# Optimization experiments

Measured on AMD Instinct MI355X. Metric: run time of the kernel, lower is better.

The kernel has to match this reference:

```python
import jax, jax.numpy as jnp
import numpy as np

# ---- static config (from xib add_argument defaults / chosen production sizes) ----
B, L = 16, 50            # batch, text length
LU, KU, DIM = 60, 100, 60
V, MAXVL = 2000, 10      # vocab size, max vocab word length (J)
MIN_WL, MAX_WL = 4, 10   # min/max extracted word length
NE = MAX_WL - MIN_WL + 1 # number of len_e candidates
INS_DEL_COST = 3.5       # min_ins_del_cost
UNEXTRACTED_PROB = 0.01
CONTEXT_WEIGHT = 0.1     # weight for context (conv) log-probs
NEG = -9999.9


def setup_inputs() -> dict:
    key = jax.random.key(0)
    ks = jax.random.split(key, 8)
    unit_id_seqs = jax.random.randint(ks[0], (B, L), 0, LU)
    lengths = 10 + jax.random.randint(ks[1], (B,), 0, L - 9)  # in [10, L]
    unit_repr = jax.random.normal(ks[2], (KU, DIM), jnp.float32)
    aligner_weight = 0.1 * jax.random.normal(ks[3], (LU, KU), jnp.float32)
    conv_w = jax.random.normal(ks[4], (DIM, DIM, 3), jnp.float32) / np.sqrt(3.0 * DIM)
    conv_b = jnp.zeros((DIM,), jnp.float32)
    vocab_ids = jax.random.randint(ks[5], (V, MAXVL), 0, KU)
    vocab_lengths = MIN_WL + jax.random.randint(ks[6], (V,), 0, MAXVL - MIN_WL + 1)
    return dict(unit_id_seqs=unit_id_seqs, lengths=lengths, unit_repr=unit_repr,
                aligner_weight=aligner_weight, conv_w=conv_w, conv_b=conv_b,
                vocab_ids=vocab_ids, vocab_lengths=vocab_lengths)


def reference(unit_id_seqs, lengths, unit_repr, aligner_weight, conv_w, conv_b,
              vocab_ids, vocab_lengths):
    # ---- G2P layer: embedding-as-matmul + Conv1d over length ----
    ku_char_repr = aligner_weight @ unit_repr                 # (LU, DIM)
    emb = ku_char_repr[unit_id_seqs]                          # (B, L, DIM)
    x = jnp.swapaxes(emb, 1, 2)                               # (B, DIM, L)
    y = jax.lax.conv_general_dilated(x, conv_w, (1,), 'SAME',
                                     dimension_numbers=('NCH', 'OIH', 'NCH'))
    word_repr = jnp.swapaxes(y + conv_b[None, :, None], 1, 2)  # (B, L, DIM)
    char_log_probs = jax.nn.log_softmax(ku_char_repr @ unit_repr.T, axis=-1)  # (LU, KU)
    alignment = jnp.exp(char_log_probs)
    ctx_log_probs = jax.nn.log_softmax(word_repr @ unit_repr.T, axis=-1)      # (B, L, KU)
    # per-position substitution log prob against each known unit
    pos_lp = char_log_probs[unit_id_seqs] + CONTEXT_WEIGHT * ctx_log_probs    # (B, L, KU)
    sub = pos_lp[:, :, vocab_ids]                                             # (B, L, V, J)
    sub = jnp.pad(sub, ((0, 0), (0, MAX_WL), (0, 0), (0, 0)), constant_values=NEG)
    J = MAXVL
    # ---- edit-distance style DP over (span char i, vocab char j), vectorized
    # over (batch, start position, vocab). prev[b,s,j,v] = f[i-1][j].
    j_ar = jnp.arange(J + 1, dtype=sub.dtype)
    prev = jnp.broadcast_to((-INS_DEL_COST * j_ar)[None, None, :, None], (B, L, J + 1, V))
    vl_idx = jnp.broadcast_to(vocab_lengths[None, None, None, :].astype(jnp.int32), (B, L, 1, V))
    lls = []
    for i in range(1, MAX_WL + 1):          # fixed small loop (<=10)
        sub_i = sub[:, i - 1:i - 1 + L]     # (B, L, V, J): char at position s+i-1
        row = [jnp.full((B, L, V), -INS_DEL_COST * i, dtype=sub.dtype)]
        for j in range(1, J + 1):           # fixed small loop (<=10)
            diag = prev[:, :, j - 1, :] + sub_i[:, :, :, j - 1]
            up = prev[:, :, j, :] - INS_DEL_COST
            left = row[j - 1] - INS_DEL_COST
            row.append(jnp.maximum(diag, jnp.maximum(up, left)))
        prev = jnp.stack(row, axis=2)       # (B, L, J+1, V)
        if i >= MIN_WL:                     # matched ll for word length i
            lls.append(jnp.take_along_axis(prev, vl_idx, axis=2)[:, :, 0, :])
    ll = jnp.stack(lls, axis=2)             # (B, L, NE, V) = matches.ll
    # ---- viability mask + unextracted penalty, pick best candidate ----
    starts = jnp.arange(L)
    word_lens = MIN_WL + jnp.arange(NE)
    viable = (starts[None, :, None] + word_lens[None, None, :]) <= lengths[:, None, None]  # (B,L,NE)
    unextracted = (lengths[:, None, None] - word_lens[None, None, :]).astype(ll.dtype)     # (B,1,NE)
    score = (ll + jnp.where(viable, 0.0, NEG)[..., None]
             + (unextracted * np.log(UNEXTRACTED_PROB))[..., None, :, None][:, 0])
    flat = score.reshape(B, L * NE * V)
    best_idx = jnp.argmax(flat, axis=1)
    best_matched_ll = jnp.max(flat, axis=1)
    start = best_idx // (NE * V)
    e_idx = (best_idx // V) % NE
    best_matched_vocab = best_idx % V
    end = start + MIN_WL + e_idx - 1
    return start, end, best_matched_ll, best_matched_vocab, alignment
```

## Files before the change

### kernel.cpp

```cpp
#include <hip/hip_runtime.h>
#include <math.h>
#include <stdint.h>

#define B_ 16
#define L_ 50
#define LU_ 60
#define KU_ 100
#define DIM_ 60
#define V_ 2000
#define MAXVL_ 10
#define MIN_WL_ 4
#define MAX_WL_ 10
#define NE_ 7
#define IDC_ 3.5f
#define LOG_UNEXT_ (-4.6051701859880913680359829093687f)
#define CTXW_ 0.1f

#define WS_KU   0
#define WS_CLP  3600
#define WS_PLP  9600
#define WS_BEST_BYTES (89600u * 4u)
#define BEST_STRIDE 8

#define URP_ 61
#define CWP_ 61

__global__ __launch_bounds__(128) void prep_kernel(
    const float* __restrict__ unit_repr,
    const float* __restrict__ aligner_weight,
    float* __restrict__ ws_f,
    unsigned long long* __restrict__ g_best,
    float* __restrict__ out_align)
{
  __shared__ float s_ur[KU_ * URP_];
  __shared__ float s_aw[KU_];
  __shared__ float s_ku[DIM_];
  __shared__ float s_lg[KU_];
  __shared__ float sred[128];
  int r = blockIdx.x;
  int t = threadIdx.x;
  if (r == 0 && t < B_) g_best[t * BEST_STRIDE] = 0ull;
  for (int i = t; i < KU_ * DIM_; i += 128)
    s_ur[(i / DIM_) * URP_ + (i % DIM_)] = unit_repr[i];
  if (t < KU_) s_aw[t] = aligner_weight[r * KU_ + t];
  __syncthreads();
  if (t < DIM_) {
    float acc = 0.f;
    for (int k = 0; k < KU_; ++k) acc += s_aw[k] * s_ur[k * URP_ + t];
    s_ku[t] = acc;
    ws_f[WS_KU + r * DIM_ + t] = acc;
  }
  __syncthreads();
  if (t < KU_) {
    float acc = 0.f;
    for (int d = 0; d < DIM_; ++d) acc += s_ku[d] * s_ur[t * URP_ + d];
    s_lg[t] = acc;
  }
  __syncthreads();
  sred[t] = (t < KU_) ? s_lg[t] : -1e30f;
  __syncthreads();
  for (int off = 64; off > 0; off >>= 1) {
    if (t < off) sred[t] = fmaxf(sred[t], sred[t + off]);
    __syncthreads();
  }
  float m = sred[0];
  __syncthreads();
  sred[t] = (t < KU_) ? expf(s_lg[t] - m) : 0.f;
  __syncthreads();
  for (int off = 64; off > 0; off >>= 1) {
    if (t < off) sred[t] += sred[t + off];
    __syncthreads();
  }
  float ls = m + logf(sred[0]);
  if (t < KU_) {
    float lp = s_lg[t] - ls;
    ws_f[WS_CLP + r * KU_ + t] = lp;
    out_align[r * KU_ + t] = expf(lp);
  }
}

__global__ __launch_bounds__(256) void ctx_kernel(
    const int* __restrict__ uid,
    const float* __restrict__ unit_repr,
    const float* __restrict__ conv_w,
    const float* __restrict__ conv_b,
    const float* __restrict__ ws_f,
    float* __restrict__ ws_plp)
{
  int bl = blockIdx.x;
  int b = bl / L_, l = bl % L_;
  int t = threadIdx.x;
  __shared__ float s_ur[KU_ * URP_];
  __shared__ float s_cw[3 * DIM_ * CWP_];
  __shared__ float sx[3 * DIM_];
  __shared__ float swr[DIM_];
  __shared__ float slog[KU_];
  __shared__ float sred[256];

  const float4* ur4 = (const float4*)unit_repr;
  for (int k = t; k < (KU_ * DIM_) / 4; k += 256) {
    float4 v = ur4[k];
    int i0 = 4 * k;
    s_ur[((i0 + 0) / DIM_) * URP_ + ((i0 + 0) % DIM_)] = v.x;
    s_ur[((i0 + 1) / DIM_) * URP_ + ((i0 + 1) % DIM_)] = v.y;
    s_ur[((i0 + 2) / DIM_) * URP_ + ((i0 + 2) % DIM_)] = v.z;
    s_ur[((i0 + 3) / DIM_) * URP_ + ((i0 + 3) % DIM_)] = v.w;
  }
  const float4* cw4 = (const float4*)conv_w;
  for (int k = t; k < (DIM_ * DIM_ * 3) / 4; k += 256) {
    float4 v = cw4[k];
    int i0 = 4 * k;
    float vv[4] = {v.x, v.y, v.z, v.w};
#pragma unroll
    for (int e = 0; e < 4; ++e) {
      int idx = i0 + e;
      int o = idx / (3 * DIM_), id = idx % (3 * DIM_);
      s_cw[id * CWP_ + o] = vv[e];
    }
  }
  if (t < 3 * DIM_) {
    int d = t / DIM_, c = t % DIM_;
    int ld = l + d - 1;
    float vv = 0.f;
    if (ld >= 0 && ld < L_) {
      int u = uid[b * L_ + ld];
      vv = ws_f[WS_KU + u * DIM_ + c];
    }
    sx[t] = vv;
  }
  __syncthreads();
  if (t < DIM_) {
    float acc = conv_b[t];
    for (int i = 0; i < DIM_; ++i) {
      acc += sx[0 * DIM_ + i] * s_cw[(i * 3 + 0) * CWP_ + t];
      acc += sx[1 * DIM_ + i] * s_cw[(i * 3 + 1) * CWP_ + t];
      acc += sx[2 * DIM_ + i] * s_cw[(i * 3 + 2) * CWP_ + t];
    }
    swr[t] = acc;
  }
  __syncthreads();
  if (t < KU_) {
    float acc = 0.f;
    for (int d = 0; d < DIM_; ++d) acc += swr[d] * s_ur[t * URP_ + d];
    slog[t] = acc;
  }
  __syncthreads();
  sred[t] = (t < KU_) ? slog[t] : -1e30f;
  __syncthreads();
  for (int off = 128; off > 0; off >>= 1) {
    if (t < off) sred[t] = fmaxf(sred[t], sred[t + off]);
    __syncthreads();
  }
  float m = sred[0];
  __syncthreads();
  sred[t] = (t < KU_) ? expf(slog[t] - m) : 0.f;
  __syncthreads();
  for (int off = 128; off > 0; off >>= 1) {
    if (t < off) sred[t] += sred[t + off];
    __syncthreads();
  }
  float ls = m + logf(sred[0]);
  if (t < KU_) {
    int u = uid[b * L_ + l];
    float lp = slog[t] - ls;
    ws_plp[bl * KU_ + t] = ws_f[WS_CLP + u * KU_ + t] + CTXW_ * lp;
  }
}

__global__ __launch_bounds__(256, 4) void dp_kernel(
    const int* __restrict__ lengths,
    const int* __restrict__ vocab_ids,
    const int* __restrict__ vocab_lengths,
    const float* __restrict__ ws_plp,
    unsigned long long* __restrict__ g_best)
{
  int bl = blockIdx.x;
  int b = bl / L_, l = bl % L_;
  int len_b = lengths[b];
  int imax = len_b - l;
  if (imax > MAX_WL_) imax = MAX_WL_;
  if (imax < MIN_WL_) return;

  __shared__ float srows[MAX_WL_ * KU_];
  __shared__ unsigned long long swave[4];
  int t = threadIdx.x;
  {
    const float4* src = (const float4*)(ws_plp + bl * KU_);
    float4* dst = (float4*)srows;
    int nf4 = imax * (KU_ / 4);
    for (int k = t; k < nf4; k += 256) dst[k] = src[k];
  }
  __syncthreads();

  int v0 = blockIdx.y * 512 + t;
  int v1 = v0 + 256;
  bool has1 = (v1 < V_);
  unsigned long long bestKey = 0ull;

  int vid0[MAXVL_], vid1[MAXVL_];
#pragma unroll
  for (int j = 0; j < MAXVL_; ++j) vid0[j] = vocab_ids[v0 * MAXVL_ + j];
  if (has1) {
#pragma unroll
    for (int j = 0; j < MAXVL_; ++j) vid1[j] = vocab_ids[v1 * MAXVL_ + j];
  } else {
#pragma unroll
    for (int j = 0; j < MAXVL_; ++j) vid1[j] = 0;
  }
  int vlen0 = vocab_lengths[v0];
  int vlen1 = has1 ? vocab_lengths[v1] : MIN_WL_;
  float prev0[MAXVL_ + 1], prev1[MAXVL_ + 1];
#pragma unroll
  for (int j = 0; j <= MAXVL_; ++j) { prev0[j] = -IDC_ * (float)j; prev1[j] = prev0[j]; }

  for (int i = 1; i <= imax; ++i) {
    const float* row = &srows[(i - 1) * KU_];
    float s0[MAXVL_], s1[MAXVL_];
#pragma unroll
    for (int j = 0; j < MAXVL_; ++j) { s0[j] = row[vid0[j]]; s1[j] = row[vid1[j]]; }
    float rowstart = -IDC_ * (float)i;
    float d0 = prev0[0], rp0 = rowstart;
    float d1 = prev1[0], rp1 = rowstart;
    prev0[0] = rowstart; prev1[0] = rowstart;
#pragma unroll
    for (int j = 1; j <= MAXVL_; ++j) {
      float t0 = fmaxf(d0 + s0[j - 1], fmaxf(prev0[j], rp0) - IDC_);
      d0 = prev0[j]; prev0[j] = t0; rp0 = t0;
      float t1 = fmaxf(d1 + s1[j - 1], fmaxf(prev1[j], rp1) - IDC_);
      d1 = prev1[j]; prev1[j] = t1; rp1 = t1;
    }
    if (i >= MIN_WL_) {
      float unext = (float)(len_b - i) * LOG_UNEXT_;
      unsigned int idx_base = (unsigned int)(l * (NE_ * V_) + (i - MIN_WL_) * V_);
      float ll0 = prev0[MIN_WL_];
#pragma unroll
      for (int jj = MIN_WL_ + 1; jj <= MAXVL_; ++jj) if (vlen0 == jj) ll0 = prev0[jj];
      {
        float score = ll0 + unext;
        unsigned int idx = idx_base + (unsigned int)v0;
        unsigned int u = __float_as_uint(score);
        u = (u & 0x80000000u) ? ~u : (u | 0x80000000u);
        unsigned long long key = ((unsigned long long)u << 32) | (unsigned long long)(~idx);
        if (key > bestKey) bestKey = key;
      }
      if (has1) {
        float ll1 = prev1[MIN_WL_];
#pragma unroll
        for (int jj = MIN_WL_ + 1; jj <= MAXVL_; ++jj) if (vlen1 == jj) ll1 = prev1[jj];
        float score = ll1 + unext;
        unsigned int idx = idx_base + (unsigned int)v1;
        unsigned int u = __float_as_uint(score);
        u = (u & 0x80000000u) ? ~u : (u | 0x80000000u);
        unsigned long long key = ((unsigned long long)u << 32) | (unsigned long long)(~idx);
        if (key > bestKey) bestKey = key;
      }
    }
  }

#pragma unroll
  for (int off = 32; off > 0; off >>= 1) {
    unsigned long long o = __shfl_down(bestKey, off);
    if (o > bestKey) bestKey = o;
  }
  int wid = t >> 6;
  if ((t & 63) == 0) swave[wid] = bestKey;
  __syncthreads();
  if (t == 0) {
    unsigned long long k0 = swave[0];
    for (int w = 1; w < 4; ++w)
      if (swave[w] > k0) k0 = swave[w];
    atomicMax(g_best + (size_t)b * BEST_STRIDE, k0);
  }
}

__global__ void decode_kernel(const unsigned long long* __restrict__ g_best,
                              float* __restrict__ out)
{
  int t = threadIdx.x;
  if (t < B_) {
    unsigned long long key = g_best[t * BEST_STRIDE];
    unsigned int u = (unsigned int)(key >> 32);
    unsigned int idx = ~((unsigned int)(key & 0xFFFFFFFFull));
    unsigned int bits = (u & 0x80000000u) ? (u & 0x7FFFFFFFu) : ~u;
    float val = __uint_as_float(bits);
    int start = (int)(idx / (NE_ * V_));
    int rem = (int)(idx % (NE_ * V_));
    int e = rem / V_;
    int vv = rem % V_;
    out[t] = (float)start;
    out[B_ + t] = (float)(start + MIN_WL_ + e - 1);
    out[2 * B_ + t] = val;
    out[3 * B_ + t] = (float)vv;
  }
}

extern "C" void kernel_launch(void* const* d_in, const int* in_sizes, int n_in,
                              void* d_out, int out_size, void* d_ws, size_t ws_size,
                              hipStream_t stream)
{
  const int* uid            = (const int*)d_in[0];
  const int* lengths        = (const int*)d_in[1];
  const float* unit_repr    = (const float*)d_in[2];
  const float* aligner_w    = (const float*)d_in[3];
  const float* conv_w       = (const float*)d_in[4];
  const float* conv_b       = (const float*)d_in[5];
  const int* vocab_ids      = (const int*)d_in[6];
  const int* vocab_lengths  = (const int*)d_in[7];
  float* out = (float*)d_out;
  float* ws_f = (float*)d_ws;
  unsigned long long* g_best =
      (unsigned long long*)((char*)d_ws + WS_BEST_BYTES);

  prep_kernel<<<LU_, 128, 0, stream>>>(unit_repr, aligner_w, ws_f, g_best,
                                       out + 4 * B_);
  ctx_kernel<<<B_ * L_, 256, 0, stream>>>(uid, unit_repr, conv_w, conv_b, ws_f,
                                          ws_f + WS_PLP);
  dim3 g3(B_ * L_, 4);
  dp_kernel<<<g3, 256, 0, stream>>>(lengths, vocab_ids, vocab_lengths,
                                    ws_f + WS_PLP, g_best);
  decode_kernel<<<1, 64, 0, stream>>>(g_best, out);
}
```

Before: 113.2 us.

## Transpose DP loop order, pack vocab ids, fuse decode via last-block counter

The edit distance DP now iterates over vocab characters in the outer loop and text positions in the inner loop. The score rows are stored transposed in shared memory, so each vocab character fetches its column with vector loads instead of ten scattered LDS reads per row. Vocab ids are packed into bytes to save registers, and each length's score is captured when j equals the vocab length. The separate decode launch is removed: the last block, found with an atomic done counter, decodes the result, which adds threadfences and an atomic per block.

New measurement: 288.4 us. +154.8%, slower.

```diff
diff --git a/kernel.cpp b/kernel.cpp
--- a/kernel.cpp
+++ b/kernel.cpp
@@ -21,15 +21,18 @@
 #define WS_PLP  9600
 #define WS_BEST_BYTES (89600u * 4u)
 #define BEST_STRIDE 8
+#define WS_DONE_BYTES (WS_BEST_BYTES + 1024u)
 
 #define URP_ 61
 #define CWP_ 61
+#define TSP_ 12
 
 __global__ __launch_bounds__(128) void prep_kernel(
     const float* __restrict__ unit_repr,
     const float* __restrict__ aligner_weight,
     float* __restrict__ ws_f,
     unsigned long long* __restrict__ g_best,
+    unsigned int* __restrict__ done_cnt,
     float* __restrict__ out_align)
 {
   __shared__ float s_ur[KU_ * URP_];
@@ -39,7 +42,10 @@
   __shared__ float sred[128];
   int r = blockIdx.x;
   int t = threadIdx.x;
-  if (r == 0 && t < B_) g_best[t * BEST_STRIDE] = 0ull;
+  if (r == 0) {
+    if (t < B_) g_best[t * BEST_STRIDE] = 0ull;
+    if (t == 0) *done_cnt = 0u;
+  }
   for (int i = t; i < KU_ * DIM_; i += 128)
     s_ur[(i / DIM_) * URP_ + (i % DIM_)] = unit_repr[i];
   if (t < KU_) s_aw[t] = aligner_weight[r * KU_ + t];
@@ -172,113 +178,140 @@
     const int* __restrict__ vocab_ids,
     const int* __restrict__ vocab_lengths,
     const float* __restrict__ ws_plp,
-    unsigned long long* __restrict__ g_best)
+    unsigned long long* __restrict__ g_best,
+    unsigned int* __restrict__ done_cnt,
+    float* __restrict__ out)
 {
   int bl = blockIdx.x;
   int b = bl / L_, l = bl % L_;
   int len_b = lengths[b];
   int imax = len_b - l;
   if (imax > MAX_WL_) imax = MAX_WL_;
-  if (imax < MIN_WL_) return;
-
-  __shared__ float srows[MAX_WL_ * KU_];
+  int t = threadIdx.x;
+  __shared__ float sT[KU_ * TSP_];
   __shared__ unsigned long long swave[4];
-  int t = threadIdx.x;
-  {
-    const float4* src = (const float4*)(ws_plp + bl * KU_);
-    float4* dst = (float4*)srows;
-    int nf4 = imax * (KU_ / 4);
-    for (int k = t; k < nf4; k += 256) dst[k] = src[k];
-  }
-  __syncthreads();
-
-  int v0 = blockIdx.y * 512 + t;
-  int v1 = v0 + 256;
-  bool has1 = (v1 < V_);
-  unsigned long long bestKey = 0ull;
-
-  int vid0[MAXVL_], vid1[MAXVL_];
-#pragma unroll
-  for (int j = 0; j < MAXVL_; ++j) vid0[j] = vocab_ids[v0 * MAXVL_ + j];
-  if (has1) {
-#pragma unroll
-    for (int j = 0; j < MAXVL_; ++j) vid1[j] = vocab_ids[v1 * MAXVL_ + j];
-  } else {
-#pragma unroll
-    for (int j = 0; j < MAXVL_; ++j) vid1[j] = 0;
-  }
-  int vlen0 = vocab_lengths[v0];
-  int vlen1 = has1 ? vocab_lengths[v1] : MIN_WL_;
-  float prev0[MAXVL_ + 1], prev1[MAXVL_ + 1];
-#pragma unroll
-  for (int j = 0; j <= MAXVL_; ++j) { prev0[j] = -IDC_ * (float)j; prev1[j] = prev0[j]; }
-
-  for (int i = 1; i <= imax; ++i) {
-    const float* row = &srows[(i - 1) * KU_];
-    float s0[MAXVL_], s1[MAXVL_];
-#pragma unroll
-    for (int j = 0; j < MAXVL_; ++j) { s0[j] = row[vid0[j]]; s1[j] = row[vid1[j]]; }
-    float rowstart = -IDC_ * (float)i;
-    float d0 = prev0[0], rp0 = rowstart;
-    float d1 = prev1[0], rp1 = rowstart;
-    prev0[0] = rowstart; prev1[0] = rowstart;
+  __shared__ int s_last;
+
+  if (imax >= MIN_WL_) {
+    int n = imax * KU_;
+    for (int idx = t; idx < n; idx += 256) {
+      int i = idx / KU_, k = idx - i * KU_;
+      sT[k * TSP_ + i] = ws_plp[(bl + i) * KU_ + k];
+    }
+    __syncthreads();
+
+    int v0 = blockIdx.y * 512 + t;
+    int v1 = v0 + 256;
+    bool has1 = (v1 < V_);
+    unsigned p0[3] = {0u, 0u, 0u}, p1[3] = {0u, 0u, 0u};
+#pragma unroll
+    for (int j = 0; j < MAXVL_; ++j)
+      p0[j >> 2] |= ((unsigned)vocab_ids[v0 * MAXVL_ + j]) << ((j & 3) * 8);
+    if (has1) {
+#pragma unroll
+      for (int j = 0; j < MAXVL_; ++j)
+        p1[j >> 2] |= ((unsigned)vocab_ids[v1 * MAXVL_ + j]) << ((j & 3) * 8);
+    }
+    int vlen0 = vocab_lengths[v0];
+    int vlen1 = has1 ? vocab_lengths[v1] : MIN_WL_;
+
+    float A0[MAXVL_ + 1], A1[MAXVL_ + 1];
+    float sv0[NE_], sv1[NE_];
+#pragma unroll
+    for (int e = 0; e < NE_; ++e) { sv0[e] = 0.f; sv1[e] = 0.f; }
+#pragma unroll
+    for (int i = 0; i <= MAXVL_; ++i) {
+      A0[i] = -IDC_ * (float)i;
+      A1[i] = A0[i];
+    }
+
 #pragma unroll
     for (int j = 1; j <= MAXVL_; ++j) {
-      float t0 = fmaxf(d0 + s0[j - 1], fmaxf(prev0[j], rp0) - IDC_);
-      d0 = prev0[j]; prev0[j] = t0; rp0 = t0;
-      float t1 = fmaxf(d1 + s1[j - 1], fmaxf(prev1[j], rp1) - IDC_);
-      d1 = prev1[j]; prev1[j] = t1; rp1 = t1;
-    }
-    if (i >= MIN_WL_) {
-      float unext = (float)(len_b - i) * LOG_UNEXT_;
-      unsigned int idx_base = (unsigned int)(l * (NE_ * V_) + (i - MIN_WL_) * V_);
-      float ll0 = prev0[MIN_WL_];
-#pragma unroll
-      for (int jj = MIN_WL_ + 1; jj <= MAXVL_; ++jj) if (vlen0 == jj) ll0 = prev0[jj];
-      {
-        float score = ll0 + unext;
-        unsigned int idx = idx_base + (unsigned int)v0;
-        unsigned int u = __float_as_uint(score);
-        u = (u & 0x80000000u) ? ~u : (u | 0x80000000u);
-        unsigned long long key = ((unsigned long long)u << 32) | (unsigned long long)(~idx);
-        if (key > bestKey) bestKey = key;
+      int k0 = (int)((p0[(j - 1) >> 2] >> (((j - 1) & 3) * 8)) & 0xFFu);
+      int k1 = (int)((p1[(j - 1) >> 2] >> (((j - 1) & 3) * 8)) & 0xFFu);
+      const float* c0 = &sT[k0 * TSP_];
+      const float* c1 = &sT[k1 * TSP_];
+      float4 a0 = *(const float4*)(c0);
+      float4 m0 = *(const float4*)(c0 + 4);
+      float2 e0 = *(const float2*)(c0 + 8);
+      float4 a1 = *(const float4*)(c1);
+      float4 m1 = *(const float4*)(c1 + 4);
+      float2 e1 = *(const float2*)(c1 + 8);
+      float s0[MAXVL_] = {a0.x, a0.y, a0.z, a0.w, m0.x, m0.y, m0.z, m0.w, e0.x, e0.y};
+      float s1[MAXVL_] = {a1.x, a1.y, a1.z, a1.w, m1.x, m1.y, m1.z, m1.w, e1.x, e1.y};
+      float B0[MAXVL_ + 1], B1[MAXVL_ + 1];
+      B0[0] = -IDC_ * (float)j;
+      B1[0] = B0[0];
+#pragma unroll
+      for (int i = 1; i <= MAXVL_; ++i) {
+        B0[i] = fmaxf(A0[i - 1] + s0[i - 1], fmaxf(A0[i], B0[i - 1]) - IDC_);
+        B1[i] = fmaxf(A1[i - 1] + s1[i - 1], fmaxf(A1[i], B1[i - 1]) - IDC_);
       }
-      if (has1) {
-        float ll1 = prev1[MIN_WL_];
-#pragma unroll
-        for (int jj = MIN_WL_ + 1; jj <= MAXVL_; ++jj) if (vlen1 == jj) ll1 = prev1[jj];
-        float score = ll1 + unext;
-        unsigned int idx = idx_base + (unsigned int)v1;
-        unsigned int u = __float_as_uint(score);
-        u = (u & 0x80000000u) ? ~u : (u | 0x80000000u);
-        unsigned long long key = ((unsigned long long)u << 32) | (unsigned long long)(~idx);
-        if (key > bestKey) bestKey = key;
+      if (j == vlen0) {
+#pragma unroll
+        for (int e = 0; e < NE_; ++e) sv0[e] = B0[MIN_WL_ + e];
       }
-    }
-  }
-
-#pragma unroll
-  for (int off = 32; off > 0; off >>= 1) {
-    unsigned long long o = __shfl_down(bestKey, off);
-    if (o > bestKey) bestKey = o;
-  }
-  int wid = t >> 6;
-  if ((t & 63) == 0) swave[wid] = bestKey;
-  __syncthreads();
+      if (j == vlen1) {
+#pragma unroll
+        for (int e = 0; e < NE_; ++e) sv1[e] = B1[MIN_WL_ + e];
+      }
+#pragma unroll
+      for (int i = 0; i <= MAXVL_; ++i) { A0[i] = B0[i]; A1[i] = B1[i]; }
+    }
+
+    unsigned long long bestKey = 0ull;
+#pragma unroll
+    for (int e = 0; e < NE_; ++e) {
+      int i = MIN_WL_ + e;
+      if (i <= imax) {
+        float unext = (float)(len_b - i) * LOG_UNEXT_;
+        unsigned int idx_base = (unsigned int)(l * (NE_ * V_) + e * V_);
+        {
+          float score = sv0[e] + unext;
+          unsigned int u = __float_as_uint(score);
+          u = (u & 0x80000000u) ? ~u : (u | 0x80000000u);
+          unsigned long long key =
+              ((unsigned long long)u << 32) |
+              (unsigned long long)(~(idx_base + (unsigned int)v0));
+          if (key > bestKey) bestKey = key;
+        }
+        if (has1) {
+          float score = sv1[e] + unext;
+          unsigned int u = __float_as_uint(score);
+          u = (u & 0x80000000u) ? ~u : (u | 0x80000000u);
+          unsigned long long key =
+              ((unsigned long long)u << 32) |
+              (unsigned long long)(~(idx_base + (unsigned int)v1));
+          if (key > bestKey) bestKey = key;
+        }
+      }
+    }
+
+#pragma unroll
+    for (int off = 32; off > 0; off >>= 1) {
+      unsigned long long o = __shfl_down(bestKey, off);
+      if (o > bestKey) bestKey = o;
+    }
+    int wid = t >> 6;
+    if ((t & 63) == 0) swave[wid] = bestKey;
+    __syncthreads();
+    if (t == 0) {
+      unsigned long long k0 = swave[0];
+      for (int w = 1; w < 4; ++w)
+        if (swave[w] > k0) k0 = swave[w];
+      atomicMax(g_best + (size_t)b * BEST_STRIDE, k0);
+    }
+  }
+
+  __threadfence();
   if (t == 0) {
-    unsigned long long k0 = swave[0];
-    for (int w = 1; w < 4; ++w)
-      if (swave[w] > k0) k0 = swave[w];
-    atomicMax(g_best + (size_t)b * BEST_STRIDE, k0);
-  }
-}
-
-__global__ void decode_kernel(const unsigned long long* __restrict__ g_best,
-                              float* __restrict__ out)
-{
-  int t = threadIdx.x;
-  if (t < B_) {
-    unsigned long long key = g_best[t * BEST_STRIDE];
+    unsigned int old = atomicAdd(done_cnt, 1u);
+    s_last = (old == gridDim.x * gridDim.y - 1u) ? 1 : 0;
+  }
+  __syncthreads();
+  if (s_last && t < B_) {
+    __threadfence();
+    unsigned long long key = atomicMax(g_best + (size_t)t * BEST_STRIDE, 0ull);
     unsigned int u = (unsigned int)(key >> 32);
     unsigned int idx = ~((unsigned int)(key & 0xFFFFFFFFull));
     unsigned int bits = (u & 0x80000000u) ? (u & 0x7FFFFFFFu) : ~u;
@@ -310,13 +343,14 @@
   float* ws_f = (float*)d_ws;
   unsigned long long* g_best =
       (unsigned long long*)((char*)d_ws + WS_BEST_BYTES);
+  unsigned int* done_cnt =
+      (unsigned int*)((char*)d_ws + WS_DONE_BYTES);
 
   prep_kernel<<<LU_, 128, 0, stream>>>(unit_repr, aligner_w, ws_f, g_best,
-                                       out + 4 * B_);
+                                       done_cnt, out + 4 * B_);
   ctx_kernel<<<B_ * L_, 256, 0, stream>>>(uid, unit_repr, conv_w, conv_b, ws_f,
                                           ws_f + WS_PLP);
   dim3 g3(B_ * L_, 4);
   dp_kernel<<<g3, 256, 0, stream>>>(lengths, vocab_ids, vocab_lengths,
-                                    ws_f + WS_PLP, g_best);
-  decode_kernel<<<1, 64, 0, stream>>>(g_best, out);
+                                    ws_f + WS_PLP, g_best, done_cnt, out);
 }
```
